# Optimization experiments

Measured on AMD Instinct MI355X. Metric: run time of the kernel, lower is better.

Reference implementation:

```python
import jax, jax.numpy as jnp
import numpy as np

N_NODES = 100000
N_EDGES = 1600000
D_FEAT = 32


def setup_inputs() -> dict:
    key = jax.random.key(0)
    kx, ke = jax.random.split(key)
    x = jax.random.normal(kx, (N_NODES, D_FEAT), dtype=jnp.float32)
    edge_index = jax.random.randint(ke, (2, N_EDGES), 0, N_NODES, dtype=jnp.int64)
    return {"x": x, "edge_index": edge_index}


def reference(x, edge_index):
    # flow='source_to_target': messages flow from edge_index[0] (j, source)
    # to edge_index[1] (i, target).
    src = edge_index[0]  # [E] source node per edge (j)
    dst = edge_index[1]  # [E] target node per edge (i)
    # __lift__: gather source-node features per edge -> message(x_j) = x_j
    msgs = jnp.take(x, src, axis=0)  # [E, D]
    # aggregate with aggr='add': scatter-sum messages onto target nodes
    out = jax.ops.segment_sum(msgs, dst, num_segments=x.shape[0])  # [N, D]
    # update: identity
    return out
```

## Files before the change

### kernel.cpp

```cpp
#include <hip/hip_runtime.h>


#define D_FEAT 32
#define BKT_SHIFT 7
#define BKT_NODES 128
#define MAX_NB 1024
#define CAPSH 5
#define ECAP 4096
#define OVFCAP 65536
typedef unsigned int u32;

__global__ void __launch_bounds__(512)
k_scatter3(const int* __restrict__ src, const int* __restrict__ dst,
           u32* __restrict__ cnt, u32* __restrict__ bin,
           u32* __restrict__ ovf, u32* __restrict__ ovf_cnt,
           int n_edges, int nb, int nsub, int chunk) {
    __shared__ u32 c_l[MAX_NB];
    int blk = blockIdx.x, t = threadIdx.x;
    for (int i = t; i < nb; i += 512) c_l[i] = 0u;
    __syncthreads();
    int beg = blk * chunk, end = min(beg + chunk, n_edges);
    for (int e = beg + t; e < end; e += 512) {
        u32 d = (u32)dst[e];
        u32 b = d >> BKT_SHIFT;
        u32 pos = atomicAdd(&c_l[b], 1u);
        u32 packed = (u32)src[e] | ((d & (BKT_NODES - 1)) << 17);
        if (pos < (1u << CAPSH)) {
            bin[(((size_t)b * nsub + blk) << CAPSH) + pos] = packed;
        } else {
            u32 g = atomicAdd(ovf_cnt, 1u);
            if (g < OVFCAP) { ovf[2 * g] = packed; ovf[2 * g + 1] = b; }
        }
    }
    __syncthreads();
    u32* row = cnt + (size_t)blk * nb;
    for (int i = t; i < nb; i += 512) row[i] = c_l[i];
}

__global__ void __launch_bounds__(512)
k_gather3(const float* __restrict__ x, const u32* __restrict__ cnt,
          const u32* __restrict__ bin, const u32* __restrict__ ovf,
          const u32* __restrict__ ovf_cnt, float* __restrict__ out,
          int n_nodes, int nb, int nsub) {
    __shared__ u32 s_cnt[512];
    __shared__ u32 s_sb[512];
    __shared__ u32 s_base[513];
    __shared__ u32 s_ent[ECAP];
    __shared__ u32 s_srt[ECAP];
    __shared__ u32 s_off[BKT_NODES + 1];
    __shared__ u32 s_cur[BKT_NODES];
    __shared__ u32 s_scan[BKT_NODES];
    int b = blockIdx.x, t = threadIdx.x;
    int node0 = b * BKT_NODES;
    const float4* x4 = (const float4*)x;
    const uint4* bin4 = (const uint4*)bin;
    int q = t & 7;
    int n0 = t >> 3;
    float4 a0 = make_float4(0.f, 0.f, 0.f, 0.f);
    float4 a1 = make_float4(0.f, 0.f, 0.f, 0.f);

    u32 c = 0u;
    if (t < nsub) c = min(cnt[(size_t)t * nb + b], 1u << CAPSH);
    s_cnt[t] = c;
    s_sb[t] = c;
    __syncthreads();
    for (int off = 1; off < 512; off <<= 1) {
        u32 y = (t >= off) ? s_sb[t - off] : 0u;
        __syncthreads();
        if (t >= off) s_sb[t] += y;
        __syncthreads();
    }
    s_base[t] = s_sb[t] - c;
    if (t == 511) s_base[512] = s_sb[511];
    __syncthreads();

    int subA = 0;
    u32 baseA = 0u;
    while (subA < nsub) {
        int lo = subA + 1, hi = nsub;
        while (lo < hi) {
            int mid = (lo + hi + 1) >> 1;
            if (s_base[mid] - baseA <= (u32)ECAP) lo = mid; else hi = mid - 1;
        }
        int subB = lo;
        int m = (int)(s_base[subB] - baseA);

        {
            int quads = (subB - subA) << (CAPSH - 2);
            size_t qbase = ((size_t)b * nsub + subA) << (CAPSH - 2);
            for (int i = t; i < quads; i += 512) {
                int sub = subA + (i >> (CAPSH - 2));
                int k4 = i & ((1 << (CAPSH - 2)) - 1);
                int slot0 = k4 << 2;
                u32 cn = s_cnt[sub];
                if ((u32)slot0 < cn) {
                    uint4 v = bin4[qbase + i];
                    u32 base = (s_base[sub] - baseA) + slot0;
                    s_ent[base] = v.x;
                    if ((u32)(slot0 + 1) < cn) s_ent[base + 1] = v.y;
                    if ((u32)(slot0 + 2) < cn) s_ent[base + 2] = v.z;
                    if ((u32)(slot0 + 3) < cn) s_ent[base + 3] = v.w;
                }
            }
        }
        if (t < BKT_NODES) s_cur[t] = 0u;
        __syncthreads();

        for (int i = t; i < m; i += 512) atomicAdd(&s_cur[s_ent[i] >> 17], 1u);
        __syncthreads();
        u32 v = 0u;
        if (t < BKT_NODES) { v = s_cur[t]; s_scan[t] = v; }
        __syncthreads();
        for (int off = 1; off < BKT_NODES; off <<= 1) {
            u32 y = 0u;
            if (t < BKT_NODES && t >= off) y = s_scan[t - off];
            __syncthreads();
            if (t < BKT_NODES && t >= off) s_scan[t] += y;
            __syncthreads();
        }
        if (t < BKT_NODES) { u32 ex = s_scan[t] - v; s_off[t] = ex; s_cur[t] = ex; }
        if (t == BKT_NODES - 1) s_off[BKT_NODES] = s_scan[BKT_NODES - 1];
        __syncthreads();
        for (int i = t; i < m; i += 512) {
            u32 p = s_ent[i];
            u32 pos = atomicAdd(&s_cur[p >> 17], 1u);
            s_srt[pos] = p & 0x1FFFFu;
        }
        __syncthreads();

        {
            u32 j = s_off[n0], j1 = s_off[n0 + 1];
            for (; j + 1 < j1; j += 2) {
                float4 xa = x4[(size_t)s_srt[j] * 8 + q];
                float4 xb = x4[(size_t)s_srt[j + 1] * 8 + q];
                a0.x += xa.x; a0.y += xa.y; a0.z += xa.z; a0.w += xa.w;
                a0.x += xb.x; a0.y += xb.y; a0.z += xb.z; a0.w += xb.w;
            }
            if (j < j1) {
                float4 xa = x4[(size_t)s_srt[j] * 8 + q];
                a0.x += xa.x; a0.y += xa.y; a0.z += xa.z; a0.w += xa.w;
            }
            j = s_off[n0 + 64]; j1 = s_off[n0 + 65];
            for (; j + 1 < j1; j += 2) {
                float4 xa = x4[(size_t)s_srt[j] * 8 + q];
                float4 xb = x4[(size_t)s_srt[j + 1] * 8 + q];
                a1.x += xa.x; a1.y += xa.y; a1.z += xa.z; a1.w += xa.w;
                a1.x += xb.x; a1.y += xb.y; a1.z += xb.z; a1.w += xb.w;
            }
            if (j < j1) {
                float4 xa = x4[(size_t)s_srt[j] * 8 + q];
                a1.x += xa.x; a1.y += xa.y; a1.z += xa.z; a1.w += xa.w;
            }
        }
        __syncthreads();
        subA = subB;
        baseA = s_base[subB];
    }

    u32 novf = min(*ovf_cnt, (u32)OVFCAP);
    for (u32 i = 0; i < novf; ++i) {
        if (ovf[2 * i + 1] == (u32)b) {
            u32 p = ovf[2 * i];
            u32 dl = p >> 17;
            if (dl == (u32)n0 || dl == (u32)(n0 + 64)) {
                float4 xv = x4[(size_t)(p & 0x1FFFFu) * 8 + q];
                if (dl == (u32)n0) { a0.x += xv.x; a0.y += xv.y; a0.z += xv.z; a0.w += xv.w; }
                else               { a1.x += xv.x; a1.y += xv.y; a1.z += xv.z; a1.w += xv.w; }
            }
        }
    }

    float4* o4 = (float4*)out;
    if (node0 + n0 < n_nodes)      o4[(size_t)node0 * 8 + t] = a0;
    if (node0 + n0 + 64 < n_nodes) o4[(size_t)node0 * 8 + 512 + t] = a1;
}


__global__ void __launch_bounds__(256)
mp_zero_kernel(float* __restrict__ out, int n) {
    int i = blockIdx.x * blockDim.x + threadIdx.x;
    if (i < n) out[i] = 0.0f;
}

__global__ void __launch_bounds__(256)
mp_scatter_kernel(const float* __restrict__ x, const int* __restrict__ src,
                  const int* __restrict__ dst, float* __restrict__ out,
                  int n_edges) {
    int idx = blockIdx.x * blockDim.x + threadIdx.x;
    if (idx >= n_edges * 8) return;
    int e = idx >> 3;
    int c = idx & 7;
    const float4 v = *reinterpret_cast<const float4*>(x + (size_t)src[e] * D_FEAT + c * 4);
    float* o = out + (size_t)dst[e] * D_FEAT + c * 4;
    unsafeAtomicAdd(o + 0, v.x);
    unsafeAtomicAdd(o + 1, v.y);
    unsafeAtomicAdd(o + 2, v.z);
    unsafeAtomicAdd(o + 3, v.w);
}


extern "C" void kernel_launch(void* const* d_in, const int* in_sizes, int n_in,
                              void* d_out, int out_size, void* d_ws, size_t ws_size,
                              hipStream_t stream) {
    const float* x = (const float*)d_in[0];
    const int* edge_index = (const int*)d_in[1];
    int n_edges = in_sizes[1] / 2;
    const int* src = edge_index;
    const int* dst = edge_index + n_edges;
    float* out = (float*)d_out;
    int n_nodes = out_size / D_FEAT;

    int nb = (n_nodes + BKT_NODES - 1) >> BKT_SHIFT;

    if (nb <= MAX_NB && n_nodes <= (1 << 17)) {
        const int ncand[3] = {512, 384, 256};
        for (int ci = 0; ci < 3; ++ci) {
            int nsub = ncand[ci];
            int chunk = (n_edges + nsub - 1) / nsub;
            size_t need = ((size_t)nsub * nb
                           + 16
                           + 2 * (size_t)OVFCAP
                           + (((size_t)nb * nsub) << CAPSH))
                          * sizeof(u32);
            if (need > ws_size) continue;

            u32* cnt     = (u32*)d_ws;
            u32* ovf_cnt = cnt + (size_t)nsub * nb;
            u32* ovf     = ovf_cnt + 16;
            u32* bin     = ovf + 2 * (size_t)OVFCAP;

            hipMemsetAsync(ovf_cnt, 0, sizeof(u32), stream);
            k_scatter3<<<nsub, 512, 0, stream>>>(src, dst, cnt, bin, ovf, ovf_cnt,
                                                 n_edges, nb, nsub, chunk);
            k_gather3<<<nb, 512, 0, stream>>>(x, cnt, bin, ovf, ovf_cnt, out,
                                              n_nodes, nb, nsub);
            return;
        }
    }

    mp_zero_kernel<<<(out_size + 255) / 256, 256, 0, stream>>>(out, out_size);
    int total_thr = n_edges * 8;
    mp_scatter_kernel<<<(total_thr + 255) / 256, 256, 0, stream>>>(x, src, dst, out, n_edges);
}
```

Before: 125.8 us.

## Stage scatter bins in LDS and write them out coalesced in sub-major layout

The scatter kernel now buffers packed edges per bucket in dynamic shared memory, then copies the whole per-block bin array to global with uint4 stores. Before, each edge was a scattered 4-byte global write. The bin layout becomes [sub][bucket][CAP] with CAP reduced from 32 to 16, and the gather kernel's indexing is updated to match. The gather accumulation loop is also unrolled to four loads per iteration to keep more memory requests in flight. The trade-offs are writing every slot, including empty ones, a heavier LDS footprint in the scatter kernel, and more overflow traffic if buckets exceed 16 entries per chunk.

```diff
diff --git a/kernel.cpp b/kernel.cpp
--- a/kernel.cpp
+++ b/kernel.cpp
@@ -4,41 +4,49 @@
 #define D_FEAT 32
 #define BKT_SHIFT 7
 #define BKT_NODES 128
-#define MAX_NB 1024
-#define CAPSH 5
+#define CAPSH 4
+#define CAP (1 << CAPSH)
 #define ECAP 4096
 #define OVFCAP 65536
 typedef unsigned int u32;
 
 __global__ void __launch_bounds__(512)
-k_scatter3(const int* __restrict__ src, const int* __restrict__ dst,
+k_scatter4(const int* __restrict__ src, const int* __restrict__ dst,
            u32* __restrict__ cnt, u32* __restrict__ bin,
            u32* __restrict__ ovf, u32* __restrict__ ovf_cnt,
            int n_edges, int nb, int nsub, int chunk) {
-    __shared__ u32 c_l[MAX_NB];
+    extern __shared__ u32 smem[];
+    u32* s_stage = smem;
+    u32* s_cur   = smem + ((size_t)nb << CAPSH);
     int blk = blockIdx.x, t = threadIdx.x;
-    for (int i = t; i < nb; i += 512) c_l[i] = 0u;
+    for (int i = t; i < nb; i += 512) s_cur[i] = 0u;
     __syncthreads();
     int beg = blk * chunk, end = min(beg + chunk, n_edges);
     for (int e = beg + t; e < end; e += 512) {
         u32 d = (u32)dst[e];
         u32 b = d >> BKT_SHIFT;
-        u32 pos = atomicAdd(&c_l[b], 1u);
+        u32 pos = atomicAdd(&s_cur[b], 1u);
         u32 packed = (u32)src[e] | ((d & (BKT_NODES - 1)) << 17);
-        if (pos < (1u << CAPSH)) {
-            bin[(((size_t)b * nsub + blk) << CAPSH) + pos] = packed;
+        if (pos < (u32)CAP) {
+            s_stage[(b << CAPSH) + pos] = packed;
         } else {
             u32 g = atomicAdd(ovf_cnt, 1u);
             if (g < OVFCAP) { ovf[2 * g] = packed; ovf[2 * g + 1] = b; }
         }
     }
     __syncthreads();
+    {
+        int nquads = (nb << CAPSH) >> 2;
+        uint4* gq = (uint4*)(bin + (((size_t)blk * nb) << CAPSH));
+        const uint4* sq = (const uint4*)s_stage;
+        for (int i = t; i < nquads; i += 512) gq[i] = sq[i];
+    }
     u32* row = cnt + (size_t)blk * nb;
-    for (int i = t; i < nb; i += 512) row[i] = c_l[i];
+    for (int i = t; i < nb; i += 512) row[i] = min(s_cur[i], (u32)CAP);
 }
 
 __global__ void __launch_bounds__(512)
-k_gather3(const float* __restrict__ x, const u32* __restrict__ cnt,
+k_gather4(const float* __restrict__ x, const u32* __restrict__ cnt,
           const u32* __restrict__ bin, const u32* __restrict__ ovf,
           const u32* __restrict__ ovf_cnt, float* __restrict__ out,
           int n_nodes, int nb, int nsub) {
@@ -60,7 +68,7 @@
     float4 a1 = make_float4(0.f, 0.f, 0.f, 0.f);
 
     u32 c = 0u;
-    if (t < nsub) c = min(cnt[(size_t)t * nb + b], 1u << CAPSH);
+    if (t < nsub) c = min(cnt[(size_t)t * nb + b], (u32)CAP);
     s_cnt[t] = c;
     s_sb[t] = c;
     __syncthreads();
@@ -87,14 +95,13 @@
 
         {
             int quads = (subB - subA) << (CAPSH - 2);
-            size_t qbase = ((size_t)b * nsub + subA) << (CAPSH - 2);
             for (int i = t; i < quads; i += 512) {
                 int sub = subA + (i >> (CAPSH - 2));
                 int k4 = i & ((1 << (CAPSH - 2)) - 1);
                 int slot0 = k4 << 2;
                 u32 cn = s_cnt[sub];
                 if ((u32)slot0 < cn) {
-                    uint4 v = bin4[qbase + i];
+                    uint4 v = bin4[(((size_t)sub * nb + b) << (CAPSH - 2)) + k4];
                     u32 base = (s_base[sub] - baseA) + slot0;
                     s_ent[base] = v.x;
                     if ((u32)(slot0 + 1) < cn) s_ent[base + 1] = v.y;
@@ -130,24 +137,32 @@
 
         {
             u32 j = s_off[n0], j1 = s_off[n0 + 1];
-            for (; j + 1 < j1; j += 2) {
+            for (; j + 3 < j1; j += 4) {
                 float4 xa = x4[(size_t)s_srt[j] * 8 + q];
                 float4 xb = x4[(size_t)s_srt[j + 1] * 8 + q];
+                float4 xc = x4[(size_t)s_srt[j + 2] * 8 + q];
+                float4 xd = x4[(size_t)s_srt[j + 3] * 8 + q];
+                a0.x += xa.x + xb.x + xc.x + xd.x;
+                a0.y += xa.y + xb.y + xc.y + xd.y;
+                a0.z += xa.z + xb.z + xc.z + xd.z;
+                a0.w += xa.w + xb.w + xc.w + xd.w;
+            }
+            for (; j < j1; ++j) {
+                float4 xa = x4[(size_t)s_srt[j] * 8 + q];
                 a0.x += xa.x; a0.y += xa.y; a0.z += xa.z; a0.w += xa.w;
-                a0.x += xb.x; a0.y += xb.y; a0.z += xb.z; a0.w += xb.w;
-            }
-            if (j < j1) {
-                float4 xa = x4[(size_t)s_srt[j] * 8 + q];
-                a0.x += xa.x; a0.y += xa.y; a0.z += xa.z; a0.w += xa.w;
             }
             j = s_off[n0 + 64]; j1 = s_off[n0 + 65];
-            for (; j + 1 < j1; j += 2) {
+            for (; j + 3 < j1; j += 4) {
                 float4 xa = x4[(size_t)s_srt[j] * 8 + q];
                 float4 xb = x4[(size_t)s_srt[j + 1] * 8 + q];
-                a1.x += xa.x; a1.y += xa.y; a1.z += xa.z; a1.w += xa.w;
-                a1.x += xb.x; a1.y += xb.y; a1.z += xb.z; a1.w += xb.w;
-            }
-            if (j < j1) {
+                float4 xc = x4[(size_t)s_srt[j + 2] * 8 + q];
+                float4 xd = x4[(size_t)s_srt[j + 3] * 8 + q];
+                a1.x += xa.x + xb.x + xc.x + xd.x;
+                a1.y += xa.y + xb.y + xc.y + xd.y;
+                a1.z += xa.z + xb.z + xc.z + xd.z;
+                a1.w += xa.w + xb.w + xc.w + xd.w;
+            }
+            for (; j < j1; ++j) {
                 float4 xa = x4[(size_t)s_srt[j] * 8 + q];
                 a1.x += xa.x; a1.y += xa.y; a1.z += xa.z; a1.w += xa.w;
             }
@@ -212,7 +227,9 @@
 
     int nb = (n_nodes + BKT_NODES - 1) >> BKT_SHIFT;
 
-    if (nb <= MAX_NB && n_nodes <= (1 << 17)) {
+    size_t sc_lds = ((size_t)nb * CAP + nb) * sizeof(u32);
+
+    if (n_nodes <= (1 << 17) && sc_lds <= 64 * 1024) {
         const int ncand[3] = {512, 384, 256};
         for (int ci = 0; ci < 3; ++ci) {
             int nsub = ncand[ci];
@@ -220,7 +237,7 @@
             size_t need = ((size_t)nsub * nb
                            + 16
                            + 2 * (size_t)OVFCAP
-                           + (((size_t)nb * nsub) << CAPSH))
+                           + (((size_t)nsub * nb) << CAPSH))
                           * sizeof(u32);
             if (need > ws_size) continue;
 
@@ -230,9 +247,9 @@
             u32* bin     = ovf + 2 * (size_t)OVFCAP;
 
             hipMemsetAsync(ovf_cnt, 0, sizeof(u32), stream);
-            k_scatter3<<<nsub, 512, 0, stream>>>(src, dst, cnt, bin, ovf, ovf_cnt,
-                                                 n_edges, nb, nsub, chunk);
-            k_gather3<<<nb, 512, 0, stream>>>(x, cnt, bin, ovf, ovf_cnt, out,
+            k_scatter4<<<nsub, 512, sc_lds, stream>>>(src, dst, cnt, bin, ovf, ovf_cnt,
+                                                      n_edges, nb, nsub, chunk);
+            k_gather4<<<nb, 512, 0, stream>>>(x, cnt, bin, ovf, ovf_cnt, out,
                                               n_nodes, nb, nsub);
             return;
         }
```

New measurement: 116.3 us. 1.08x faster.
